# Optimization experiments

Hardware: AMD Instinct MI355X
Metric: run time of the kernel (lower is better)

The kernel has to match this reference:

```python
import jax, jax.numpy as jnp
import numpy as np

D = 1536          # d_model
H = 12            # n_heads // 2 for chunk attention
HD = D // H       # head dim = 128
MAXC = 256        # max_chunks
MAXLEN = 1024     # max_seq_length (size embedding table)
THRESH = 0.5      # boundary threshold (init value of the learned param)


def _gelu(v):
    return jax.nn.gelu(v, approximate=False)  # torch nn.GELU default (erf)


def _cos(a, b):
    # F.cosine_similarity with eps=1e-8
    na = jnp.maximum(jnp.linalg.norm(a, axis=-1), 1e-8)
    nb = jnp.maximum(jnp.linalg.norm(b, axis=-1), 1e-8)
    return jnp.sum(a * b, axis=-1) / (na * nb)


def _interp1d(y, L_out):
    # F.interpolate(mode='linear', align_corners=False) on [B, L_in] -> [B, L_out]
    L_in = y.shape[1]
    src = jnp.clip((jnp.arange(L_out, dtype=y.dtype) + 0.5) * (L_in / L_out) - 0.5, 0.0, L_in - 1)
    i0 = jnp.floor(src).astype(jnp.int32)
    i1 = jnp.minimum(i0 + 1, L_in - 1)
    w = src - i0.astype(y.dtype)
    return y[:, i0] * (1.0 - w) + y[:, i1] * w


def setup_inputs() -> dict:
    key = jax.random.key(0)
    ks = jax.random.split(key, 16)
    B, S = 4, 1024
    rn = lambda k, sh, s=0.02: jax.random.normal(k, sh, dtype=jnp.float32) * s
    return {
        'x': jax.random.normal(ks[0], (B, S, D), dtype=jnp.float32),
        'Wp': rn(ks[1], (D, D)), 'bp': jnp.zeros((D,), jnp.float32),
        'detW1': rn(ks[2], (3, D, 2 * D)), 'detb1': jnp.zeros((3, D), jnp.float32),
        'detW2': rn(ks[3], (3, D // 2, D)), 'detb2': jnp.zeros((3, D // 2), jnp.float32),
        'detW3': rn(ks[4], (3, D // 2)), 'detb3': jnp.zeros((3,), jnp.float32),
        'in_proj_w': rn(ks[5], (3 * D, D)), 'in_proj_b': jnp.zeros((3 * D,), jnp.float32),
        'out_w': rn(ks[6], (D, D)), 'out_b': jnp.zeros((D,), jnp.float32),
        'size_emb': jax.random.normal(ks[7], (MAXLEN, D), dtype=jnp.float32),
        'pos_enc': rn(ks[8], (1, MAXC, D)),
        'procW1': rn(ks[9], (2 * D, D)), 'procb1': jnp.zeros((2 * D,), jnp.float32),
        'procW2': rn(ks[10], (D, 2 * D)), 'procb2': jnp.zeros((D,), jnp.float32),
        'ln_g': jnp.ones((D,), jnp.float32), 'ln_b': jnp.zeros((D,), jnp.float32),
    }


def reference(x, Wp, bp, detW1, detb1, detW2, detb2, detW3, detb3,
              in_proj_w, in_proj_b, out_w, out_b, size_emb, pos_enc,
              procW1, procb1, procW2, procb2, ln_g, ln_b):
    B, S, d = x.shape
    # ---- DynamicSemanticChunker ----
    x_ling = x @ Wp.T + bp
    sims = []
    for scale in (1, 2, 4):
        xs = x_ling[:, ::scale]
        cs = _cos(xs[:, :-1], xs[:, 1:])           # [B, L-1]
        sims.append(_interp1d(cs, S - 1))           # [B, S-1]
    avg_sim = jnp.mean(jnp.stack(sims, 0), axis=0)
    base = 0.5 * (1.0 - avg_sim)
    bi = jnp.concatenate([x[:, :-1], x[:, 1:]], axis=-1)  # [B, S-1, 2d]
    h1 = _gelu(jnp.einsum('bsk,ndk->nbsd', bi, detW1) + detb1[:, None, None, :])
    h2 = _gelu(jnp.einsum('nbsd,nhd->nbsh', h1, detW2) + detb2[:, None, None, :])
    learned = jax.nn.sigmoid(jnp.einsum('nbsh,nh->nbs', h2, detW3) + detb3[:, None, None])
    avg_learned = jnp.mean(learned, axis=0)
    final = 0.6 * base + 0.4 * avg_learned
    boundaries = jnp.concatenate([jnp.ones((B, 1), x.dtype), final], axis=1)  # [B, S]
    # ---- EnhancedChunkLayer.create_chunks ----
    # contiguous ragged chunks == segments between boundary positions
    seg = jnp.cumsum((boundaries > THRESH).astype(jnp.int32), axis=1) - 1      # [B, S]
    # per-chunk MHA == full-seq attention with block-diagonal same-segment mask
    qkv = x @ in_proj_w.T + in_proj_b
    q, k, v = jnp.split(qkv, 3, axis=-1)
    q = q.reshape(B, S, H, HD)
    k = k.reshape(B, S, H, HD)
    v = v.reshape(B, S, H, HD)
    scores = jnp.einsum('bqhd,bkhd->bhqk', q, k) / np.sqrt(HD).astype(np.float32)
    same = (seg[:, None, :, None] == seg[:, None, None, :])                    # [B,1,S,S]
    scores = jnp.where(same, scores, jnp.asarray(-1e9, scores.dtype))
    attn = jax.nn.softmax(scores, axis=-1)
    ctx = jnp.einsum('bhqk,bkhd->bqhd', attn, v).reshape(B, S, d)
    attn_out = ctx @ out_w.T + out_b                                           # [B, S, d]
    # masked segment mean pooling; chunks with id >= MAXC are truncated away
    onehot = (seg[..., None] == jnp.arange(MAXC)).astype(x.dtype)              # [B,S,MAXC]
    sums = jnp.einsum('bsm,bsd->bmd', onehot, attn_out)
    counts = jnp.sum(onehot, axis=1)                                            # [B,MAXC]
    mean = sums / jnp.maximum(counts, 1.0)[..., None]
    clen = jnp.minimum(counts.astype(jnp.int32), MAXLEN - 1)
    sizes = size_emb[clen]                                                      # [B,MAXC,d]
    chunk = jnp.where(counts[..., None] > 0, mean + sizes, 0.0)                 # zero-pad empty
    # ---- pos encoding + chunk_processor (Linear->GELU->Linear->LayerNorm) ----
    chunk = chunk + pos_enc
    h = _gelu(chunk @ procW1.T + procb1)
    y = h @ procW2.T + procb2
    mu = jnp.mean(y, axis=-1, keepdims=True)
    var = jnp.var(y, axis=-1, keepdims=True)
    y = (y - mu) / jnp.sqrt(var + 1e-5) * ln_g + ln_b
    return y  # [B, MAXC, d]
```

## Files before the change

### kernel.cpp

```cpp
#include <hip/hip_runtime.h>
#include <hip/hip_bf16.h>
#include <math.h>

#define D_ 1536
#define S_ 1024
#define B_ 4
#define H_ 12
#define HD_ 128
#define MAXC_ 256

typedef __bf16 bf16x8_t __attribute__((ext_vector_type(8)));
typedef float f32x4_t __attribute__((ext_vector_type(4)));

__device__ __forceinline__ float gelu_f(float v) {
    return 0.5f * v * (1.0f + erff(v / 1.41421356237f));
}

__device__ __forceinline__ void split2(float a, __hip_bfloat16& h, __hip_bfloat16& l) {
    h = __float2bfloat16(a);
    l = __float2bfloat16(a - __bfloat162float(h));
}

__device__ __forceinline__ void xcd_swizzle(int& bx, int& by, int gx, int gy) {
    int nwg = gx * gy;
    int orig = by * gx + bx;
    int xcd = orig & 7;
    int q = nwg >> 3, r = nwg & 7;
    int wg = (xcd < r ? xcd * (q + 1) : r * (q + 1) + (xcd - r) * q) + (orig >> 3);
    bx = wg % gx;
    by = wg / gx;
}

template<int BM, int SPLITA, int SPLITB, int ACT, int OUT, int DBUF>
__global__ __launch_bounds__(256, 2)
void mfma3_gemm(const float* __restrict__ Af, const __hip_bfloat16* __restrict__ Ah,
                const __hip_bfloat16* __restrict__ Al,
                const float* __restrict__ Bf, const __hip_bfloat16* __restrict__ Bh,
                const __hip_bfloat16* __restrict__ Bl,
                const float* __restrict__ bias, int biasStride,
                float* __restrict__ Cf, __hip_bfloat16* __restrict__ Ch, __hip_bfloat16* __restrict__ Cl,
                const float* __restrict__ w3, float* __restrict__ lg,
                int K, int lda, int ldb, int ldc,
                long long aBound, long long azS, long long bzS, long long czS)
{
    constexpr int NB = DBUF ? 2 : 1;
    __shared__ __align__(16) __hip_bfloat16 Ash[NB][BM * 32], Asl[NB][BM * 32];
    __shared__ __align__(16) __hip_bfloat16 Bsh[NB][128 * 32], Bsl[NB][128 * 32];
    const int z = blockIdx.z;
    int bxi = blockIdx.x, byi = blockIdx.y;
    xcd_swizzle(bxi, byi, gridDim.x, gridDim.y);
    const int bm = byi * BM, bn = bxi * 128;
    const int tid = threadIdx.x, lane = tid & 63, wave = tid >> 6;
    const int wm = (BM == 128) ? (wave >> 1) : 0;
    const int wn = (BM == 128) ? (wave & 1) : wave;
    constexpr int NF = (BM == 128) ? 4 : 2;
    constexpr int WC = NF * 16;
    const int fr = lane & 15, kg = lane >> 4;
    f32x4_t acc[4][NF] = {};
    constexpr int RSH = (BM == 128) ? 1 : 2;
    constexpr int NBA = (BM == 128) ? 2 : 1;
    const int ar = tid >> RSH, akb = tid & ((1 << RSH) - 1);
    const int br = tid >> 1, bkb = tid & 1;

    bf16x8_t rAh[NBA], rAl[NBA], rBh[2], rBl[2];
    float4 rAf[NBA][2], rBf[2][2];

    auto load_tile = [&](int k0) {
        #pragma unroll
        for (int j = 0; j < NBA; ++j) {
            int skg = akb * NBA + j;
            long long base = (long long)(bm + ar) * lda + azS * z + k0 + skg * 8;
            if (SPLITA) {
                #pragma unroll
                for (int q = 0; q < 2; ++q) {
                    float4 v = make_float4(0.f, 0.f, 0.f, 0.f);
                    if (base + q * 4 + 4 <= aBound) v = *reinterpret_cast<const float4*>(&Af[base + q * 4]);
                    rAf[j][q] = v;
                }
            } else {
                rAh[j] = *reinterpret_cast<const bf16x8_t*>(&Ah[base]);
                rAl[j] = *reinterpret_cast<const bf16x8_t*>(&Al[base]);
            }
        }
        #pragma unroll
        for (int j = 0; j < 2; ++j) {
            int skg = bkb * 2 + j;
            long long base = (long long)(bn + br) * ldb + bzS * z + k0 + skg * 8;
            if (SPLITB) {
                #pragma unroll
                for (int q = 0; q < 2; ++q)
                    rBf[j][q] = *reinterpret_cast<const float4*>(&Bf[base + q * 4]);
            } else {
                rBh[j] = *reinterpret_cast<const bf16x8_t*>(&Bh[base]);
                rBl[j] = *reinterpret_cast<const bf16x8_t*>(&Bl[base]);
            }
        }
    };

    auto write_tile = [&](int buf) {
        #pragma unroll
        for (int j = 0; j < NBA; ++j) {
            int skg = akb * NBA + j;
            int blk = ar * 4 + (skg ^ ((ar >> 1) & 3));
            if (SPLITA) {
                float av[8];
                *reinterpret_cast<float4*>(&av[0]) = rAf[j][0];
                *reinterpret_cast<float4*>(&av[4]) = rAf[j][1];
                __hip_bfloat16 hh[8], ll[8];
                #pragma unroll
                for (int q = 0; q < 8; ++q) split2(av[q], hh[q], ll[q]);
                *reinterpret_cast<bf16x8_t*>(&Ash[buf][blk * 8]) = *reinterpret_cast<bf16x8_t*>(hh);
                *reinterpret_cast<bf16x8_t*>(&Asl[buf][blk * 8]) = *reinterpret_cast<bf16x8_t*>(ll);
            } else {
                *reinterpret_cast<bf16x8_t*>(&Ash[buf][blk * 8]) = rAh[j];
                *reinterpret_cast<bf16x8_t*>(&Asl[buf][blk * 8]) = rAl[j];
            }
        }
        #pragma unroll
        for (int j = 0; j < 2; ++j) {
            int skg = bkb * 2 + j;
            int blk = br * 4 + (skg ^ ((br >> 1) & 3));
            if (SPLITB) {
                float av[8];
                *reinterpret_cast<float4*>(&av[0]) = rBf[j][0];
                *reinterpret_cast<float4*>(&av[4]) = rBf[j][1];
                __hip_bfloat16 hh[8], ll[8];
                #pragma unroll
                for (int q = 0; q < 8; ++q) split2(av[q], hh[q], ll[q]);
                *reinterpret_cast<bf16x8_t*>(&Bsh[buf][blk * 8]) = *reinterpret_cast<bf16x8_t*>(hh);
                *reinterpret_cast<bf16x8_t*>(&Bsl[buf][blk * 8]) = *reinterpret_cast<bf16x8_t*>(ll);
            } else {
                *reinterpret_cast<bf16x8_t*>(&Bsh[buf][blk * 8]) = rBh[j];
                *reinterpret_cast<bf16x8_t*>(&Bsl[buf][blk * 8]) = rBl[j];
            }
        }
    };

    load_tile(0);
    write_tile(0);
    __syncthreads();
    int cur = 0;

    for (int k0 = 0; k0 < K; k0 += 32) {
        const bool has_next = (k0 + 32) < K;
        if (has_next) load_tile(k0 + 32);

        bf16x8_t fah[4], fal[4], fbh[NF], fbl[NF];
        #pragma unroll
        for (int m = 0; m < 4; ++m) {
            int row = wm * 64 + m * 16 + fr;
            int blk = row * 4 + (kg ^ ((row >> 1) & 3));
            fah[m] = *reinterpret_cast<const bf16x8_t*>(&Ash[cur][blk * 8]);
            fal[m] = *reinterpret_cast<const bf16x8_t*>(&Asl[cur][blk * 8]);
        }
        #pragma unroll
        for (int n = 0; n < NF; ++n) {
            int row = wn * WC + n * 16 + fr;
            int blk = row * 4 + (kg ^ ((row >> 1) & 3));
            fbh[n] = *reinterpret_cast<const bf16x8_t*>(&Bsh[cur][blk * 8]);
            fbl[n] = *reinterpret_cast<const bf16x8_t*>(&Bsl[cur][blk * 8]);
        }
        #pragma unroll
        for (int m = 0; m < 4; ++m)
            #pragma unroll
            for (int n = 0; n < NF; ++n) {
                acc[m][n] = __builtin_amdgcn_mfma_f32_16x16x32_bf16(fah[m], fbh[n], acc[m][n], 0, 0, 0);
                acc[m][n] = __builtin_amdgcn_mfma_f32_16x16x32_bf16(fah[m], fbl[n], acc[m][n], 0, 0, 0);
                acc[m][n] = __builtin_amdgcn_mfma_f32_16x16x32_bf16(fal[m], fbh[n], acc[m][n], 0, 0, 0);
            }

        if (has_next) {
            if (DBUF) {
                write_tile(cur ^ 1);
                __syncthreads();
                cur ^= 1;
            } else {
                __syncthreads();
                write_tile(0);
                __syncthreads();
            }
        }
    }

    const int fq = lane >> 4;
    const float* bp_ = bias + (long long)biasStride * z;

    if constexpr (OUT == 2) {
        float psum[4][4] = {};
        #pragma unroll
        for (int n = 0; n < NF; ++n) {
            int col = bn + wn * WC + n * 16 + fr;
            float bv = bp_[col];
            float wv = w3[(long long)biasStride * z + col];
            #pragma unroll
            for (int m = 0; m < 4; ++m)
                #pragma unroll
                for (int r = 0; r < 4; ++r) {
                    float v = acc[m][n][r] + bv;
                    v = gelu_f(v);
                    psum[m][r] += v * wv;
                }
        }
        #pragma unroll
        for (int m = 0; m < 4; ++m)
            #pragma unroll
            for (int r = 0; r < 4; ++r) {
                float p = psum[m][r];
                p += __shfl_xor(p, 1);
                p += __shfl_xor(p, 2);
                p += __shfl_xor(p, 4);
                p += __shfl_xor(p, 8);
                if (fr == 0) {
                    int row = bm + wm * 64 + m * 16 + fq * 4 + r;
                    atomicAdd(&lg[czS * z + row], p);
                }
            }
        return;
    }

    #pragma unroll
    for (int n = 0; n < NF; ++n) {
        int col = bn + wn * WC + n * 16 + fr;
        float bv = bp_[col];
        #pragma unroll
        for (int m = 0; m < 4; ++m) {
            int row0 = bm + wm * 64 + m * 16 + fq * 4;
            #pragma unroll
            for (int r = 0; r < 4; ++r) {
                float v = acc[m][n][r] + bv;
                if (ACT == 1) v = gelu_f(v);
                long long ci = czS * z + (long long)(row0 + r) * ldc + col;
                if constexpr (OUT == 0) {
                    Cf[ci] = v;
                } else {
                    __hip_bfloat16 hh, ll;
                    split2(v, hh, ll);
                    Ch[ci] = hh; Cl[ci] = ll;
                }
            }
        }
    }
}

template<int ACT, int OUT_BF16>
__global__ __launch_bounds__(256)
void mfma_gemm(const __hip_bfloat16* __restrict__ A, const __hip_bfloat16* __restrict__ Bw,
               const float* __restrict__ bias, void* __restrict__ Cout,
               int M, int N, int K)
{
    __shared__ __align__(16) __hip_bfloat16 As[128 * 32];
    __shared__ __align__(16) __hip_bfloat16 Bs[128 * 32];
    const int tid = threadIdx.x;
    const int lane = tid & 63;
    const int wave = tid >> 6;
    const int wm = wave >> 1, wn = wave & 1;
    int bxi = blockIdx.x, byi = blockIdx.y;
    xcd_swizzle(bxi, byi, gridDim.x, gridDim.y);
    const int bm = byi * 128, bn = bxi * 128;
    const int fr = lane & 15, kg = lane >> 4;

    f32x4_t acc[4][4] = {};

    auto stage = [&](int k0) {
        #pragma unroll
        for (int c = 0; c < 2; ++c) {
            int idx = (wave * 2 + c) * 64 + lane;
            int row = idx >> 2, slot = idx & 3;
            int srck = slot ^ ((row >> 1) & 3);
            const __hip_bfloat16* ga = &A[(long long)(bm + row) * K + k0 + srck * 8];
            const __hip_bfloat16* gb = &Bw[(long long)(bn + row) * K + k0 + srck * 8];
            __builtin_amdgcn_global_load_lds(
                (const __attribute__((address_space(1))) unsigned int*)ga,
                (__attribute__((address_space(3))) unsigned int*)&As[(wave * 2 + c) * 512],
                16, 0, 0);
            __builtin_amdgcn_global_load_lds(
                (const __attribute__((address_space(1))) unsigned int*)gb,
                (__attribute__((address_space(3))) unsigned int*)&Bs[(wave * 2 + c) * 512],
                16, 0, 0);
        }
    };

    for (int k0 = 0; k0 < K; k0 += 32) {
        stage(k0);
        __syncthreads();

        bf16x8_t af[4], bfr[4];
        #pragma unroll
        for (int m = 0; m < 4; ++m) {
            int row = wm * 64 + m * 16 + fr;
            af[m] = *reinterpret_cast<const bf16x8_t*>(&As[(row * 4 + (kg ^ ((row >> 1) & 3))) * 8]);
        }
        #pragma unroll
        for (int n = 0; n < 4; ++n) {
            int row = wn * 64 + n * 16 + fr;
            bfr[n] = *reinterpret_cast<const bf16x8_t*>(&Bs[(row * 4 + (kg ^ ((row >> 1) & 3))) * 8]);
        }
        #pragma unroll
        for (int m = 0; m < 4; ++m)
            #pragma unroll
            for (int n = 0; n < 4; ++n)
                acc[m][n] = __builtin_amdgcn_mfma_f32_16x16x32_bf16(af[m], bfr[n], acc[m][n], 0, 0, 0);

        __syncthreads();
    }
    const int fq = lane >> 4;
    #pragma unroll
    for (int n = 0; n < 4; ++n) {
        int col = bn + wn * 64 + n * 16 + fr;
        float bv = bias[col];
        #pragma unroll
        for (int m = 0; m < 4; ++m) {
            int row0 = bm + wm * 64 + m * 16 + fq * 4;
            #pragma unroll
            for (int r = 0; r < 4; ++r) {
                float v = acc[m][n][r] + bv;
                if (ACT == 1) v = gelu_f(v);
                if (OUT_BF16) ((__hip_bfloat16*)Cout)[(long long)(row0 + r) * N + col] = __float2bfloat16(v);
                else          ((float*)Cout)[(long long)(row0 + r) * N + col] = v;
            }
        }
    }
}

__global__ __launch_bounds__(256)
void f2b_kernel(const float* __restrict__ in, __hip_bfloat16* __restrict__ out, int n4)
{
    int i = blockIdx.x * 256 + threadIdx.x;
    if (i >= n4) return;
    float4 v = reinterpret_cast<const float4*>(in)[i];
    __hip_bfloat16 h[4] = { __float2bfloat16(v.x), __float2bfloat16(v.y),
                            __float2bfloat16(v.z), __float2bfloat16(v.w) };
    reinterpret_cast<short4*>(out)[i] = *reinterpret_cast<short4*>(h);
}

__global__ __launch_bounds__(256)
void split_kernel(const float* __restrict__ in, __hip_bfloat16* __restrict__ oh,
                  __hip_bfloat16* __restrict__ ol, int n4)
{
    int i = blockIdx.x * 256 + threadIdx.x;
    if (i >= n4) return;
    float4 v = reinterpret_cast<const float4*>(in)[i];
    __hip_bfloat16 h[4], l[4];
    split2(v.x, h[0], l[0]); split2(v.y, h[1], l[1]);
    split2(v.z, h[2], l[2]); split2(v.w, h[3], l[3]);
    reinterpret_cast<short4*>(oh)[i] = *reinterpret_cast<short4*>(h);
    reinterpret_cast<short4*>(ol)[i] = *reinterpret_cast<short4*>(l);
}

__global__ __launch_bounds__(64)
void cs_kernel(const float* __restrict__ xl, float* __restrict__ cs)
{
    int idx = blockIdx.x;
    int b = blockIdx.y;
    int sc, i, off;
    if (idx < 1023)      { sc = 1; i = idx;        off = 0;    }
    else if (idx < 1534) { sc = 2; i = idx - 1023; off = 1023; }
    else                 { sc = 4; i = idx - 1534; off = 1534; }
    const float* ra = xl + ((long long)b * S_ + (long long)i * sc) * D_;
    const float* rb = ra + (long long)sc * D_;
    int lane = threadIdx.x;
    float dp = 0.f, na = 0.f, nb = 0.f;
    for (int d = lane; d < D_; d += 64) {
        float a = ra[d], c = rb[d];
        dp += a * c; na += a * a; nb += c * c;
    }
    #pragma unroll
    for (int o = 32; o; o >>= 1) {
        dp += __shfl_down(dp, o);
        na += __shfl_down(na, o);
        nb += __shfl_down(nb, o);
    }
    if (lane == 0) {
        float den = fmaxf(sqrtf(na), 1e-8f) * fmaxf(sqrtf(nb), 1e-8f);
        cs[(long long)b * 1789 + off + i] = dp / den;
    }
}

__global__ void final_kernel(const float* __restrict__ cs, const float* __restrict__ logits,
                             const float* __restrict__ b3, float* __restrict__ fin)
{
    int g = blockIdx.x * blockDim.x + threadIdx.x;
    if (g >= B_ * 1023) return;
    int b = g / 1023, t = g % 1023;
    const float* c = cs + (long long)b * 1789;
    float v0 = c[t];
    const float r2 = (float)(511.0 / 1023.0);
    float src2 = fminf(fmaxf(((float)t + 0.5f) * r2 - 0.5f, 0.0f), 510.0f);
    int i0 = (int)floorf(src2);
    int i1 = min(i0 + 1, 510);
    float w2 = src2 - (float)i0;
    float v1 = c[1023 + i0] * (1.0f - w2) + c[1023 + i1] * w2;
    const float r4 = (float)(255.0 / 1023.0);
    float src4 = fminf(fmaxf(((float)t + 0.5f) * r4 - 0.5f, 0.0f), 254.0f);
    int j0 = (int)floorf(src4);
    int j1 = min(j0 + 1, 254);
    float w4 = src4 - (float)j0;
    float v2 = c[1534 + j0] * (1.0f - w4) + c[1534 + j1] * w4;
    float avg = ((v0 + v1) + v2) / 3.0f;
    float base = 0.5f * (1.0f - avg);
    int rr = b * 1024 + t;
    float l0 = 1.0f / (1.0f + expf(-(logits[0 * 4096 + rr] + b3[0])));
    float l1 = 1.0f / (1.0f + expf(-(logits[1 * 4096 + rr] + b3[1])));
    float l2 = 1.0f / (1.0f + expf(-(logits[2 * 4096 + rr] + b3[2])));
    float al = ((l0 + l1) + l2) / 3.0f;
    fin[g] = 0.6f * base + 0.4f * al;
}

__global__ __launch_bounds__(64)
void seg_kernel(const float* __restrict__ fin, int* __restrict__ seg)
{
    int b = blockIdx.x;
    int lane = threadIdx.x;
    int loc[16];
    int cnt = 0;
    #pragma unroll
    for (int i = 0; i < 16; ++i) {
        int t = lane * 16 + i;
        int v = (t >= 1 && fin[b * 1023 + t - 1] > 0.5f) ? 1 : 0;
        cnt += v;
        loc[i] = cnt;
    }
    int inc = cnt;
    #pragma unroll
    for (int o = 1; o < 64; o <<= 1) {
        int u = __shfl_up(inc, o);
        if (lane >= o) inc += u;
    }
    int ex = inc - cnt;
    #pragma unroll
    for (int i = 0; i < 16; ++i) {
        int t = lane * 16 + i;
        seg[b * S_ + t] = ex + loc[i];
    }
}

__global__ void segrange_kernel(const float* __restrict__ fin, const int* __restrict__ seg,
                                int* __restrict__ sstart, int* __restrict__ send,
                                int* __restrict__ cfirst, int* __restrict__ ccount)
{
    int gs = blockIdx.x * blockDim.x + threadIdx.x;
    if (gs >= B_ * S_) return;
    int b = gs / S_, s = gs % S_;
    const float* f = fin + b * 1023;
    int t = s;
    while (t > 0 && !(f[t - 1] > 0.5f)) --t;
    int e = s;
    while (e < 1023 && !(f[e] > 0.5f)) ++e;
    sstart[gs] = t;
    send[gs] = e + 1;
    if (s == t) {
        int m = seg[gs];
        if (m < MAXC_) { cfirst[b * MAXC_ + m] = t; ccount[b * MAXC_ + m] = e + 1 - t; }
    }
}

__global__ __launch_bounds__(256)
void attn_kernel(const __hip_bfloat16* __restrict__ qkv, const int* __restrict__ sstart,
                 const int* __restrict__ send, __hip_bfloat16* __restrict__ ctx)
{
    int gs = blockIdx.x;
    int h = blockIdx.y * 4 + threadIdx.y;
    int lane = threadIdx.x;
    int b = gs >> 10;
    const __hip_bfloat16* qrow = qkv + (long long)gs * 4608 + h * HD_;
    float q0 = __bfloat162float(qrow[lane]), q1 = __bfloat162float(qrow[lane + 64]);
    int st = sstart[gs], en = send[gs];
    float m = -INFINITY, l = 0.f, a0 = 0.f, a1 = 0.f;
    for (int t = st; t < en; ++t) {
        long long krow = ((long long)(b * S_ + t)) * 4608 + 1536 + h * HD_;
        float p = q0 * __bfloat162float(qkv[krow + lane]) + q1 * __bfloat162float(qkv[krow + lane + 64]);
        #pragma unroll
        for (int o = 32; o; o >>= 1) p += __shfl_xor(p, o);
        p = p / 11.3137084989847603904f;
        float nm = fmaxf(m, p);
        float scale = expf(m - nm);
        float w = expf(p - nm);
        long long vrow = ((long long)(b * S_ + t)) * 4608 + 3072 + h * HD_;
        l = l * scale + w;
        a0 = a0 * scale + w * __bfloat162float(qkv[vrow + lane]);
        a1 = a1 * scale + w * __bfloat162float(qkv[vrow + lane + 64]);
        m = nm;
    }
    float inv = 1.0f / l;
    ctx[(long long)gs * D_ + h * HD_ + lane] = __float2bfloat16(a0 * inv);
    ctx[(long long)gs * D_ + h * HD_ + lane + 64] = __float2bfloat16(a1 * inv);
}

__global__ __launch_bounds__(256)
void chunk_kernel(const float* __restrict__ attn_out, const int* __restrict__ cfirst,
                  const int* __restrict__ ccount, const float* __restrict__ size_emb,
                  const float* __restrict__ pos_enc, __hip_bfloat16* __restrict__ chunk)
{
    int m = blockIdx.x, b = blockIdx.y;
    int cnt = ccount[b * MAXC_ + m];
    for (int d = threadIdx.x; d < D_; d += 256) {
        float v;
        if (cnt > 0) {
            int first = cfirst[b * MAXC_ + m];
            float ssum = 0.f;
            for (int t = 0; t < cnt; ++t)
                ssum += attn_out[((long long)(b * S_ + first + t)) * D_ + d];
            float mean = ssum / (float)cnt;
            int clen = min(cnt, 1023);
            v = mean + size_emb[(long long)clen * D_ + d];
        } else {
            v = 0.f;
        }
        v += pos_enc[m * D_ + d];
        chunk[((long long)(b * MAXC_ + m)) * D_ + d] = __float2bfloat16(v);
    }
}

__global__ __launch_bounds__(256)
void ln_kernel(const float* __restrict__ y0, const float* __restrict__ g,
               const float* __restrict__ bb, float* __restrict__ out)
{
    int r = blockIdx.x;
    const float* row = y0 + (long long)r * D_;
    float loc[6];
    float s = 0.f;
    #pragma unroll
    for (int i = 0; i < 6; ++i) { loc[i] = row[threadIdx.x + i * 256]; s += loc[i]; }
    __shared__ float red[256];
    red[threadIdx.x] = s; __syncthreads();
    for (int o = 128; o; o >>= 1) { if (threadIdx.x < o) red[threadIdx.x] += red[threadIdx.x + o]; __syncthreads(); }
    float mu = red[0] / 1536.0f;
    __syncthreads();
    float s2 = 0.f;
    #pragma unroll
    for (int i = 0; i < 6; ++i) { float d = loc[i] - mu; s2 += d * d; }
    red[threadIdx.x] = s2; __syncthreads();
    for (int o = 128; o; o >>= 1) { if (threadIdx.x < o) red[threadIdx.x] += red[threadIdx.x + o]; __syncthreads(); }
    float var = red[0] / 1536.0f;
    float inv = 1.0f / sqrtf(var + 1e-5f);
    #pragma unroll
    for (int i = 0; i < 6; ++i) {
        int d = threadIdx.x + i * 256;
        out[(long long)r * D_ + d] = (loc[i] - mu) * inv * g[d] + bb[d];
    }
}

extern "C" void kernel_launch(void* const* d_in, const int* in_sizes, int n_in,
                              void* d_out, int out_size, void* d_ws, size_t ws_size,
                              hipStream_t stream)
{
    const float* x         = (const float*)d_in[0];
    const float* Wp        = (const float*)d_in[1];
    const float* bp        = (const float*)d_in[2];
    const float* detW1     = (const float*)d_in[3];
    const float* detb1     = (const float*)d_in[4];
    const float* detW2     = (const float*)d_in[5];
    const float* detb2     = (const float*)d_in[6];
    const float* detW3     = (const float*)d_in[7];
    const float* detb3     = (const float*)d_in[8];
    const float* in_proj_w = (const float*)d_in[9];
    const float* in_proj_b = (const float*)d_in[10];
    const float* out_w     = (const float*)d_in[11];
    const float* out_b     = (const float*)d_in[12];
    const float* size_emb  = (const float*)d_in[13];
    const float* pos_enc   = (const float*)d_in[14];
    const float* procW1    = (const float*)d_in[15];
    const float* procb1    = (const float*)d_in[16];
    const float* procW2    = (const float*)d_in[17];
    const float* procb2    = (const float*)d_in[18];
    const float* ln_g      = (const float*)d_in[19];
    const float* ln_b      = (const float*)d_in[20];
    float* out = (float*)d_out;

    const bool big = ws_size >= (size_t)192 * 1024 * 1024;

    char* ws = (char*)d_ws;
    float*          xlingf = (float*)(ws + 0);
    __hip_bfloat16* Wph    = (__hip_bfloat16*)(ws + 25165824);
    __hip_bfloat16* Wpl    = (__hip_bfloat16*)(ws + 29884416);
    __hip_bfloat16* h1h    = (__hip_bfloat16*)(ws + 0);
    __hip_bfloat16* h1l    = (__hip_bfloat16*)(ws + 37748736);
    __hip_bfloat16* W1h_s  = (__hip_bfloat16*)(ws + 75497472);
    __hip_bfloat16* W1l_s  = (__hip_bfloat16*)(ws + 94371840);
    __hip_bfloat16* W2h_s  = (__hip_bfloat16*)(ws + 75497472);
    __hip_bfloat16* W2l_s  = (__hip_bfloat16*)(ws + 82575360);
    __hip_bfloat16* xh     = (__hip_bfloat16*)(ws + 75497472);
    __hip_bfloat16* xl     = (__hip_bfloat16*)(ws + 88082432);
    __hip_bfloat16* W1h_b  = (__hip_bfloat16*)(ws + 125829120);
    __hip_bfloat16* W1l_b  = (__hip_bfloat16*)(ws + 154140672);
    __hip_bfloat16* W2h_b  = (__hip_bfloat16*)(ws + 125829120);
    __hip_bfloat16* W2l_b  = (__hip_bfloat16*)(ws + 132907008);
    __hip_bfloat16* xb_s       = (__hip_bfloat16*)(ws + 0);
    __hip_bfloat16* in_proj_wb = (__hip_bfloat16*)(ws + 12582912);
    __hip_bfloat16* qkvb       = (__hip_bfloat16*)(ws + 26738688);
    __hip_bfloat16* ctxb       = (__hip_bfloat16*)(ws + 64487424);
    __hip_bfloat16* out_wb     = (__hip_bfloat16*)(ws + 12582912);
    float*          attno      = (float*)(ws + 77070336);
    __hip_bfloat16* chunkb     = (__hip_bfloat16*)(ws + 0);
    __hip_bfloat16* procW1b    = (__hip_bfloat16*)(ws + 3145728);
    __hip_bfloat16* hmidb      = (__hip_bfloat16*)(ws + 12582912);
    __hip_bfloat16* procW2b    = (__hip_bfloat16*)(ws + 18874368);
    float*          y0         = (float*)(ws + 28311552);
    char* sm = ws + 113246208;
    float* csb    = (float*)(sm + 0);
    float* logits = (float*)(sm + 28672);
    float* fin    = (float*)(sm + 77824);
    int*   seg    = (int*)  (sm + 94208);
    int*   sstart = (int*)  (sm + 110592);
    int*   send   = (int*)  (sm + 126976);
    int*   cfirst = (int*)  (sm + 143360);
    int*   ccount = (int*)  (sm + 147456);

    const long long SLICE_W1 = 4718592LL;
    const long long SLICE_W2 = 1179648LL;
    const long long H1_Z     = 6291456LL;

    split_kernel<<<(2359296 / 4 + 255) / 256, 256, 0, stream>>>(Wp, Wph, Wpl, 2359296 / 4);
    if (big)
        split_kernel<<<(6291456 / 4 + 255) / 256, 256, 0, stream>>>(x, xh, xl, 6291456 / 4);

    if (big)
        mfma3_gemm<128, 0, 0, 0, 0, 1><<<dim3(12, 32, 1), 256, 0, stream>>>(
            nullptr, xh, xl, nullptr, Wph, Wpl, bp, 0,
            xlingf, nullptr, nullptr, nullptr, nullptr,
            1536, 1536, 1536, 1536, 0LL, 0LL, 0LL, 0LL);
    else
        mfma3_gemm<64, 1, 0, 0, 0, 1><<<dim3(12, 64, 1), 256, 0, stream>>>(
            x, nullptr, nullptr, nullptr, Wph, Wpl, bp, 0,
            xlingf, nullptr, nullptr, nullptr, nullptr,
            1536, 1536, 1536, 1536, 6291456LL, 0LL, 0LL, 0LL);
    cs_kernel<<<dim3(1789, 4), 64, 0, stream>>>(xlingf, csb);

    if (big) {
        split_kernel<<<(14155776 / 4 + 255) / 256, 256, 0, stream>>>(detW1, W1h_b, W1l_b, 14155776 / 4);
        mfma3_gemm<128, 0, 0, 1, 1, 0><<<dim3(12, 32, 3), 256, 0, stream>>>(
            nullptr, xh, xl, nullptr, W1h_b, W1l_b, detb1, 1536,
            nullptr, h1h, h1l, nullptr, nullptr,
            3072, 1536, 3072, 1536, 0LL, 0LL, SLICE_W1, H1_Z);
    } else {
        split_kernel<<<(2 * 4718592 / 4 + 255) / 256, 256, 0, stream>>>(detW1, W1h_s, W1l_s, 2 * 4718592 / 4);
        mfma3_gemm<128, 1, 0, 1, 1, 0><<<dim3(12, 32, 2), 256, 0, stream>>>(
            x, nullptr, nullptr, nullptr, W1h_s, W1l_s, detb1, 1536,
            nullptr, h1h, h1l, nullptr, nullptr,
            3072, 1536, 3072, 1536, 6291456LL, 0LL, SLICE_W1, H1_Z);
        split_kernel<<<(4718592 / 4 + 255) / 256, 256, 0, stream>>>(detW1 + 2 * SLICE_W1, W1h_s, W1l_s, 4718592 / 4);
        mfma3_gemm<64, 1, 0, 1, 1, 0><<<dim3(12, 64, 1), 256, 0, stream>>>(
            x, nullptr, nullptr, nullptr, W1h_s, W1l_s, detb1 + 2 * 1536, 1536,
            nullptr, h1h + 2 * H1_Z, h1l + 2 * H1_Z, nullptr, nullptr,
            3072, 1536, 3072, 1536, 6291456LL, 0LL, 0LL, 0LL);
    }

    __hip_bfloat16* W2h = big ? W2h_b : W2h_s;
    __hip_bfloat16* W2l = big ? W2l_b : W2l_s;
    split_kernel<<<(3538944 / 4 + 255) / 256, 256, 0, stream>>>(detW2, W2h, W2l, 3538944 / 4);
    hipMemsetAsync(logits, 0, 3 * 4096 * sizeof(float), stream);
    mfma3_gemm<128, 0, 0, 1, 2, 1><<<dim3(6, 32, 3), 256, 0, stream>>>(
        nullptr, h1h, h1l, nullptr, W2h, W2l, detb2, 768,
        nullptr, nullptr, nullptr, detW3, logits,
        1536, 1536, 1536, 768, 0LL, H1_Z, SLICE_W2, 4096LL);

    final_kernel<<<16, 256, 0, stream>>>(csb, logits, detb3, fin);
    seg_kernel<<<4, 64, 0, stream>>>(fin, seg);
    hipMemsetAsync(ccount, 0, B_ * MAXC_ * sizeof(int), stream);
    segrange_kernel<<<16, 256, 0, stream>>>(fin, seg, sstart, send, cfirst, ccount);

    const __hip_bfloat16* xbf;
    if (big) {
        xbf = xh;
    } else {
        f2b_kernel<<<(4096 * 1536 / 4 + 255) / 256, 256, 0, stream>>>(x, xb_s, 4096 * 1536 / 4);
        xbf = xb_s;
    }
    f2b_kernel<<<(4608 * 1536 / 4 + 255) / 256, 256, 0, stream>>>(in_proj_w, in_proj_wb, 4608 * 1536 / 4);
    mfma_gemm<0, 1><<<dim3(36, 32), 256, 0, stream>>>(xbf, in_proj_wb, in_proj_b, qkvb, 4096, 4608, 1536);

    attn_kernel<<<dim3(4096, 3), dim3(64, 4), 0, stream>>>(qkvb, sstart, send, ctxb);

    f2b_kernel<<<(1536 * 1536 / 4 + 255) / 256, 256, 0, stream>>>(out_w, out_wb, 1536 * 1536 / 4);
    mfma_gemm<0, 0><<<dim3(12, 32), 256, 0, stream>>>(ctxb, out_wb, out_b, attno, 4096, 1536, 1536);

    chunk_kernel<<<dim3(256, 4), 256, 0, stream>>>(attno, cfirst, ccount, size_emb, pos_enc, chunkb);

    f2b_kernel<<<(3072 * 1536 / 4 + 255) / 256, 256, 0, stream>>>(procW1, procW1b, 3072 * 1536 / 4);
    mfma_gemm<1, 1><<<dim3(24, 8), 256, 0, stream>>>(chunkb, procW1b, procb1, hmidb, 1024, 3072, 1536);
    f2b_kernel<<<(1536 * 3072 / 4 + 255) / 256, 256, 0, stream>>>(procW2, procW2b, 1536 * 3072 / 4);
    mfma_gemm<0, 0><<<dim3(12, 8), 256, 0, stream>>>(hmidb, procW2b, procb2, y0, 1024, 1536, 3072);

    ln_kernel<<<1024, 256, 0, stream>>>(y0, ln_g, ln_b, out);
}
```

Before: 1.069 ms.

## Add direct global-to-LDS split-bf16 GEMM kernel for big-workspace path

Introduces a 128x128 three-pass split-bf16 MFMA GEMM that stages A/B tiles into shared memory with global_load_lds, using an XOR swizzle to avoid bank conflicts. It replaces the previous register-staged, optionally double-buffered kernel for the Wp, detW1 and detW2 GEMMs when the large workspace is available. The aim is to cut VGPR pressure and the issue cost of moving tiles through registers. In exchange, the new kernel is single-buffered with two barriers per K step and does not overlap loads with MFMA work.

```diff
diff --git a/kernel.cpp b/kernel.cpp
--- a/kernel.cpp
+++ b/kernel.cpp
@@ -29,6 +29,141 @@
     int wg = (xcd < r ? xcd * (q + 1) : r * (q + 1) + (xcd - r) * q) + (orig >> 3);
     bx = wg % gx;
     by = wg / gx;
+}
+
+template<int ACT, int OUT>
+__global__ __launch_bounds__(256, 2)
+void mfma3_glds(const __hip_bfloat16* __restrict__ Ah, const __hip_bfloat16* __restrict__ Al,
+                const __hip_bfloat16* __restrict__ Bh, const __hip_bfloat16* __restrict__ Bl,
+                const float* __restrict__ bias, int biasStride,
+                float* __restrict__ Cf, __hip_bfloat16* __restrict__ Ch, __hip_bfloat16* __restrict__ Cl,
+                const float* __restrict__ w3, float* __restrict__ lg,
+                int K, int lda, int ldb, int ldc,
+                long long azS, long long bzS, long long czS)
+{
+    __shared__ __align__(16) __hip_bfloat16 Ash[128 * 32], Asl[128 * 32];
+    __shared__ __align__(16) __hip_bfloat16 Bsh[128 * 32], Bsl[128 * 32];
+    const int z = blockIdx.z;
+    int bxi = blockIdx.x, byi = blockIdx.y;
+    xcd_swizzle(bxi, byi, gridDim.x, gridDim.y);
+    const int bm = byi * 128, bn = bxi * 128;
+    const int tid = threadIdx.x, lane = tid & 63, wave = tid >> 6;
+    const int wm = wave >> 1, wn = wave & 1;
+    const int fr = lane & 15, kg = lane >> 4;
+    f32x4_t acc[4][4] = {};
+
+    auto stage = [&](int k0) {
+        #pragma unroll
+        for (int c = 0; c < 2; ++c) {
+            int idx = (wave * 2 + c) * 64 + lane;
+            int row = idx >> 2, slot = idx & 3;
+            int srck = slot ^ ((row >> 1) & 3);
+            long long abase = (long long)(bm + row) * lda + azS * z + k0 + srck * 8;
+            long long bbase = (long long)(bn + row) * ldb + bzS * z + k0 + srck * 8;
+            int dst = (wave * 2 + c) * 512;
+            __builtin_amdgcn_global_load_lds(
+                (const __attribute__((address_space(1))) unsigned int*)&Ah[abase],
+                (__attribute__((address_space(3))) unsigned int*)&Ash[dst], 16, 0, 0);
+            __builtin_amdgcn_global_load_lds(
+                (const __attribute__((address_space(1))) unsigned int*)&Al[abase],
+                (__attribute__((address_space(3))) unsigned int*)&Asl[dst], 16, 0, 0);
+            __builtin_amdgcn_global_load_lds(
+                (const __attribute__((address_space(1))) unsigned int*)&Bh[bbase],
+                (__attribute__((address_space(3))) unsigned int*)&Bsh[dst], 16, 0, 0);
+            __builtin_amdgcn_global_load_lds(
+                (const __attribute__((address_space(1))) unsigned int*)&Bl[bbase],
+                (__attribute__((address_space(3))) unsigned int*)&Bsl[dst], 16, 0, 0);
+        }
+    };
+
+    for (int k0 = 0; k0 < K; k0 += 32) {
+        stage(k0);
+        __syncthreads();
+
+        bf16x8_t fah[4], fal[4], fbh[4], fbl[4];
+        #pragma unroll
+        for (int m = 0; m < 4; ++m) {
+            int row = wm * 64 + m * 16 + fr;
+            int blk = row * 4 + (kg ^ ((row >> 1) & 3));
+            fah[m] = *reinterpret_cast<const bf16x8_t*>(&Ash[blk * 8]);
+            fal[m] = *reinterpret_cast<const bf16x8_t*>(&Asl[blk * 8]);
+        }
+        #pragma unroll
+        for (int n = 0; n < 4; ++n) {
+            int row = wn * 64 + n * 16 + fr;
+            int blk = row * 4 + (kg ^ ((row >> 1) & 3));
+            fbh[n] = *reinterpret_cast<const bf16x8_t*>(&Bsh[blk * 8]);
+            fbl[n] = *reinterpret_cast<const bf16x8_t*>(&Bsl[blk * 8]);
+        }
+        #pragma unroll
+        for (int m = 0; m < 4; ++m)
+            #pragma unroll
+            for (int n = 0; n < 4; ++n) {
+                acc[m][n] = __builtin_amdgcn_mfma_f32_16x16x32_bf16(fah[m], fbh[n], acc[m][n], 0, 0, 0);
+                acc[m][n] = __builtin_amdgcn_mfma_f32_16x16x32_bf16(fah[m], fbl[n], acc[m][n], 0, 0, 0);
+                acc[m][n] = __builtin_amdgcn_mfma_f32_16x16x32_bf16(fal[m], fbh[n], acc[m][n], 0, 0, 0);
+            }
+        __syncthreads();
+    }
+
+    const int fq = lane >> 4;
+    const float* bp_ = bias + (long long)biasStride * z;
+
+    if constexpr (OUT == 2) {
+        float psum[4][4] = {};
+        #pragma unroll
+        for (int n = 0; n < 4; ++n) {
+            int col = bn + wn * 64 + n * 16 + fr;
+            float bv = bp_[col];
+            float wv = w3[(long long)biasStride * z + col];
+            #pragma unroll
+            for (int m = 0; m < 4; ++m)
+                #pragma unroll
+                for (int r = 0; r < 4; ++r) {
+                    float v = acc[m][n][r] + bv;
+                    v = gelu_f(v);
+                    psum[m][r] += v * wv;
+                }
+        }
+        #pragma unroll
+        for (int m = 0; m < 4; ++m)
+            #pragma unroll
+            for (int r = 0; r < 4; ++r) {
+                float p = psum[m][r];
+                p += __shfl_xor(p, 1);
+                p += __shfl_xor(p, 2);
+                p += __shfl_xor(p, 4);
+                p += __shfl_xor(p, 8);
+                if (fr == 0) {
+                    int row = bm + wm * 64 + m * 16 + fq * 4 + r;
+                    atomicAdd(&lg[czS * z + row], p);
+                }
+            }
+        return;
+    }
+
+    #pragma unroll
+    for (int n = 0; n < 4; ++n) {
+        int col = bn + wn * 64 + n * 16 + fr;
+        float bv = bp_[col];
+        #pragma unroll
+        for (int m = 0; m < 4; ++m) {
+            int row0 = bm + wm * 64 + m * 16 + fq * 4;
+            #pragma unroll
+            for (int r = 0; r < 4; ++r) {
+                float v = acc[m][n][r] + bv;
+                if (ACT == 1) v = gelu_f(v);
+                long long ci = czS * z + (long long)(row0 + r) * ldc + col;
+                if constexpr (OUT == 0) {
+                    Cf[ci] = v;
+                } else {
+                    __hip_bfloat16 hh, ll;
+                    split2(v, hh, ll);
+                    Ch[ci] = hh; Cl[ci] = ll;
+                }
+            }
+        }
+    }
 }
 
 template<int BM, int SPLITA, int SPLITB, int ACT, int OUT, int DBUF>
@@ -615,10 +750,10 @@
         split_kernel<<<(6291456 / 4 + 255) / 256, 256, 0, stream>>>(x, xh, xl, 6291456 / 4);
 
     if (big)
-        mfma3_gemm<128, 0, 0, 0, 0, 1><<<dim3(12, 32, 1), 256, 0, stream>>>(
-            nullptr, xh, xl, nullptr, Wph, Wpl, bp, 0,
+        mfma3_glds<0, 0><<<dim3(12, 32, 1), 256, 0, stream>>>(
+            xh, xl, Wph, Wpl, bp, 0,
             xlingf, nullptr, nullptr, nullptr, nullptr,
-            1536, 1536, 1536, 1536, 0LL, 0LL, 0LL, 0LL);
+            1536, 1536, 1536, 1536, 0LL, 0LL, 0LL);
     else
         mfma3_gemm<64, 1, 0, 0, 0, 1><<<dim3(12, 64, 1), 256, 0, stream>>>(
             x, nullptr, nullptr, nullptr, Wph, Wpl, bp, 0,
@@ -628,10 +763,10 @@
 
     if (big) {
         split_kernel<<<(14155776 / 4 + 255) / 256, 256, 0, stream>>>(detW1, W1h_b, W1l_b, 14155776 / 4);
-        mfma3_gemm<128, 0, 0, 1, 1, 0><<<dim3(12, 32, 3), 256, 0, stream>>>(
-            nullptr, xh, xl, nullptr, W1h_b, W1l_b, detb1, 1536,
+        mfma3_glds<1, 1><<<dim3(12, 32, 3), 256, 0, stream>>>(
+            xh, xl, W1h_b, W1l_b, detb1, 1536,
             nullptr, h1h, h1l, nullptr, nullptr,
-            3072, 1536, 3072, 1536, 0LL, 0LL, SLICE_W1, H1_Z);
+            3072, 1536, 3072, 1536, 0LL, SLICE_W1, H1_Z);
     } else {
         split_kernel<<<(2 * 4718592 / 4 + 255) / 256, 256, 0, stream>>>(detW1, W1h_s, W1l_s, 2 * 4718592 / 4);
         mfma3_gemm<128, 1, 0, 1, 1, 0><<<dim3(12, 32, 2), 256, 0, stream>>>(
@@ -649,10 +784,16 @@
     __hip_bfloat16* W2l = big ? W2l_b : W2l_s;
     split_kernel<<<(3538944 / 4 + 255) / 256, 256, 0, stream>>>(detW2, W2h, W2l, 3538944 / 4);
     hipMemsetAsync(logits, 0, 3 * 4096 * sizeof(float), stream);
-    mfma3_gemm<128, 0, 0, 1, 2, 1><<<dim3(6, 32, 3), 256, 0, stream>>>(
-        nullptr, h1h, h1l, nullptr, W2h, W2l, detb2, 768,
-        nullptr, nullptr, nullptr, detW3, logits,
-        1536, 1536, 1536, 768, 0LL, H1_Z, SLICE_W2, 4096LL);
+    if (big)
+        mfma3_glds<1, 2><<<dim3(6, 32, 3), 256, 0, stream>>>(
+            h1h, h1l, W2h, W2l, detb2, 768,
+            nullptr, nullptr, nullptr, detW3, logits,
+            1536, 1536, 1536, 768, H1_Z, SLICE_W2, 4096LL);
+    else
+        mfma3_gemm<128, 0, 0, 1, 2, 1><<<dim3(6, 32, 3), 256, 0, stream>>>(
+            nullptr, h1h, h1l, nullptr, W2h, W2l, detb2, 768,
+            nullptr, nullptr, nullptr, detW3, logits,
+            1536, 1536, 1536, 768, 0LL, H1_Z, SLICE_W2, 4096LL);
 
     final_kernel<<<16, 256, 0, stream>>>(csb, logits, detb3, fin);
     seg_kernel<<<4, 64, 0, stream>>>(fin, seg);
```

Result: no change. 1.090 ms (+2.0%).
